# Performance work log

Measured on AMD Instinct MI355X. Metric: run time of the kernel, lower is better.

## Reference

```python
import jax, jax.numpy as jnp
import numpy as np
from jax import lax

DIM = 1024
INTER = 512
N_EXPERTS = 16
TOPK = 4
ROUTE_SCALE = 2.5
VOCAB = 32000


def setup_inputs() -> dict:
    key = jax.random.key(0)
    ks = jax.random.split(key, 8)
    x = jax.random.normal(ks[0], (2, 512, DIM), dtype=jnp.float32)
    input_ids = jax.random.randint(ks[1], (2, 512), 0, VOCAB)
    s = 0.02
    gate_w = jax.random.normal(ks[2], (N_EXPERTS, DIM), dtype=jnp.float32) * s
    gate_b = jax.random.normal(ks[3], (N_EXPERTS,), dtype=jnp.float32) * s
    # routed experts: w13 maps dim -> 2*inter (gate|up), w2 maps inter -> dim
    w13 = jax.random.normal(ks[4], (N_EXPERTS, 2 * INTER, DIM), dtype=jnp.float32) * s
    w2 = jax.random.normal(ks[5], (N_EXPERTS, DIM, INTER), dtype=jnp.float32) * s
    # shared expert
    w13_s = jax.random.normal(ks[6], (2 * INTER, DIM), dtype=jnp.float32) * s
    w2_s = jax.random.normal(ks[7], (DIM, INTER), dtype=jnp.float32) * s
    return {"x": x, "input_ids": input_ids, "gate_w": gate_w, "gate_b": gate_b,
            "w13": w13, "w2": w2, "w13_s": w13_s, "w2_s": w2_s}


def _silu_and_mul(gu):
    gate, up = jnp.split(gu, 2, axis=-1)
    return jax.nn.silu(gate) * up


def reference(x, input_ids, gate_w, gate_b, w13, w2, w13_s, w2_s):
    B, S, D = x.shape
    xt = x.reshape(-1, D)                      # [T, D]
    T = xt.shape[0]
    # ---- Gate (sigmoid score func, bias added for selection only) ----
    scores = jax.nn.sigmoid(xt.astype(jnp.float32) @ gate_w.T)   # [T, E]
    biased = scores + gate_b
    _, idx = lax.top_k(biased, TOPK)                             # [T, K] int
    w = jnp.take_along_axis(scores, idx, axis=-1)                # [T, K]
    w = w / jnp.sum(w, axis=-1, keepdims=True)                   # normalize (non-softmax)
    w = w * ROUTE_SCALE
    # ---- dispatch/combine as dense per-expert combine weights ----
    comb = jnp.zeros((T, N_EXPERTS), jnp.float32)
    comb = comb.at[jnp.arange(T)[:, None], idx].add(w)           # [T, E]
    comb = comb.astype(x.dtype)

    def expert_body(y, args):
        w13_e, w2_e, c_e = args                                  # [2I,D], [D,I], [T]
        h = _silu_and_mul(xt @ w13_e.T)                          # [T, I]
        return y + c_e[:, None] * (h @ w2_e.T), None

    y, _ = lax.scan(expert_body, jnp.zeros_like(xt), (w13, w2, comb.T))
    # ---- shared expert ----
    y = y + _silu_and_mul(xt @ w13_s.T) @ w2_s.T
    return y.astype(x.dtype).reshape(B, S, D)
```

## Files before the change

kernel.cpp:

```cpp
#include <hip/hip_runtime.h>
#include <hip/hip_bf16.h>
#include <math.h>

#define NTOK   1024
#define DIMX   1024
#define INTERX 512
#define NEXP   16
#define RSCALE 2.5f

typedef _Float16 f16x8 __attribute__((ext_vector_type(8)));
typedef _Float16 f16x4v __attribute__((ext_vector_type(4)));
typedef float    f32x4 __attribute__((ext_vector_type(4)));

#define N_W13  (NEXP * 2 * INTERX * DIMX)
#define N_W2   (NEXP * DIMX * INTERX)
#define N_W13S (2 * INTERX * DIMX)
#define N_W2S  (DIMX * INTERX)
#define N_X    (NTOK * DIMX)
#define N_CVTW ((size_t)N_W13 + N_W2 + N_W13S + N_W2S)
#define N_CVT  (N_CVTW + N_X)

#define WS_COUNTS  0
#define WS_TOKIDX  256
#define WS_SLOTS   (WS_TOKIDX + NEXP * NTOK * 4)
#define WS_WQ      (WS_SLOTS + NTOK * 16)
#define WS_SEL     (WS_WQ + NTOK * 16)
#define WS_NT      (WS_SEL + NTOK * 16)
#define WS_TE      (WS_NT + 64)
#define WS_TM      (WS_TE + 1024)
#define WS_TR      (WS_TM + 1024)
#define WS_H       (WS_TR + 1024)
#define WS_YC      (WS_H + (size_t)5120 * 512 * 2)
#define WS_F16     (WS_YC + (size_t)5120 * 1024 * 4)

#define SWZ(r, k) ((r) * 64 + ((k) ^ (((r) & 7) << 3)))

#define GATE_BLOCKS 256
#define CVTW_BLOCKS 3264

__device__ __forceinline__ f16x8 ldcvt(const float* __restrict__ p) {
    const float4 a = *(const float4*)p;
    const float4 b = *(const float4*)(p + 4);
    return (f16x8){(_Float16)a.x, (_Float16)a.y, (_Float16)a.z, (_Float16)a.w,
                   (_Float16)b.x, (_Float16)b.y, (_Float16)b.z, (_Float16)b.w};
}

__device__ __forceinline__ void gl_lds16(const _Float16* g, _Float16* l) {
    __builtin_amdgcn_global_load_lds(
        (const __attribute__((address_space(1))) void*)g,
        (__attribute__((address_space(3))) void*)l, 16, 0, 0);
}

__global__ __launch_bounds__(256) void gate_cvt(
    const float* __restrict__ x, const float* __restrict__ gw,
    const float* __restrict__ gb,
    const float* __restrict__ w13, const float* __restrict__ w2,
    const float* __restrict__ w13s, const float* __restrict__ w2s,
    int* __restrict__ sel, float* __restrict__ wq,
    _Float16* __restrict__ dh, _Float16* __restrict__ xh)
{
    if (blockIdx.x >= GATE_BLOCKS) {
        const size_t base8 = (size_t)(blockIdx.x - GATE_BLOCKS) * 256 + threadIdx.x;
        float4 ra[4], rb[4];
#pragma unroll
        for (int it = 0; it < 4; ++it) {
            size_t off = (base8 + (size_t)it * (CVTW_BLOCKS * 256)) * 8;
            const float* s;
            if (off < N_W13)                       s = w13 + off;
            else if ((off -= N_W13) < N_W2)        s = w2 + off;
            else if ((off -= N_W2) < N_W13S)       s = w13s + off;
            else                                   s = w2s + (off - N_W13S);
            ra[it] = *(const float4*)s;
            rb[it] = *(const float4*)(s + 4);
        }
#pragma unroll
        for (int it = 0; it < 4; ++it) {
            const size_t i8 = base8 + (size_t)it * (CVTW_BLOCKS * 256);
            f16x8 v = {(_Float16)ra[it].x, (_Float16)ra[it].y,
                       (_Float16)ra[it].z, (_Float16)ra[it].w,
                       (_Float16)rb[it].x, (_Float16)rb[it].y,
                       (_Float16)rb[it].z, (_Float16)rb[it].w};
            *(f16x8*)(dh + i8 * 8) = v;
        }
        return;
    }

    const int t    = blockIdx.x * 4 + (threadIdx.x >> 6);
    const int lane = threadIdx.x & 63;
    const int e    = lane & 15;
    const int q    = lane >> 4;

    const float4* xq = (const float4*)(x + (size_t)t * DIMX) + q * 64;
    const float4* gq = (const float4*)(gw + (size_t)e * DIMX) + q * 64;
    float s0 = 0.f, s1 = 0.f, s2 = 0.f, s3 = 0.f;
#pragma unroll 8
    for (int i = 0; i < 64; i += 2) {
        const float4 a = xq[i],     b = gq[i];
        const float4 c = xq[i + 1], d = gq[i + 1];
        s0 = fmaf(a.x, b.x, s0); s1 = fmaf(a.y, b.y, s1);
        s2 = fmaf(a.z, b.z, s2); s3 = fmaf(a.w, b.w, s3);
        s0 = fmaf(c.x, d.x, s0); s1 = fmaf(c.y, d.y, s1);
        s2 = fmaf(c.z, d.z, s2); s3 = fmaf(c.w, d.w, s3);
    }
    float acc = (s0 + s1) + (s2 + s3);
    acc += __shfl_xor(acc, 16);
    acc += __shfl_xor(acc, 32);

    {
        const float* xr = x + (size_t)t * DIMX + lane * 16;
        *(f16x8*)(xh + (size_t)t * DIMX + lane * 16)     = ldcvt(xr);
        *(f16x8*)(xh + (size_t)t * DIMX + lane * 16 + 8) = ldcvt(xr + 8);
    }

    const float sv = 1.f / (1.f + __expf(-acc));
    float v = (lane < 16) ? (sv + gb[e]) : -1e30f;

    float wk0, wk1, wk2, wk3; int ek0, ek1, ek2, ek3;
    float wsum = 0.f;
#pragma unroll
    for (int k = 0; k < 4; ++k) {
        float bestv = v; int besti = lane;
#pragma unroll
        for (int off = 8; off >= 1; off >>= 1) {
            const float ov = __shfl_xor(bestv, off);
            const int   oi = __shfl_xor(besti, off);
            if (ov > bestv || (ov == bestv && oi < besti)) { bestv = ov; besti = oi; }
        }
        besti = __shfl(besti, 0);
        const float sbest = __shfl(sv, besti);
        if (k == 0) { wk0 = sbest; ek0 = besti; }
        if (k == 1) { wk1 = sbest; ek1 = besti; }
        if (k == 2) { wk2 = sbest; ek2 = besti; }
        if (k == 3) { wk3 = sbest; ek3 = besti; }
        wsum += sbest;
        if (lane == besti) v = -1e30f;
    }
    const float scale = RSCALE / wsum;

    if (lane == 0) {
        sel[t * 4 + 0] = ek0;  wq[t * 4 + 0] = wk0 * scale;
        sel[t * 4 + 1] = ek1;  wq[t * 4 + 1] = wk1 * scale;
        sel[t * 4 + 2] = ek2;  wq[t * 4 + 2] = wk2 * scale;
        sel[t * 4 + 3] = ek3;  wq[t * 4 + 3] = wk3 * scale;
    }
}

__global__ __launch_bounds__(1024) void build(
    const int* __restrict__ sel,
    int* __restrict__ counts, int* __restrict__ tok_idx,
    int* __restrict__ slots,
    int* __restrict__ n_tiles, int* __restrict__ tile_e,
    int* __restrict__ tile_m0, int* __restrict__ tile_r0)
{
    __shared__ int lc[NEXP];
    const int t = threadIdx.x;
    if (t < NEXP) lc[t] = 0;
    __syncthreads();

    int e0 = sel[t * 4 + 0], e1 = sel[t * 4 + 1];
    int e2 = sel[t * 4 + 2], e3 = sel[t * 4 + 3];
    int p0 = atomicAdd(&lc[e0], 1);
    int p1 = atomicAdd(&lc[e1], 1);
    int p2 = atomicAdd(&lc[e2], 1);
    int p3 = atomicAdd(&lc[e3], 1);
    tok_idx[e0 * NTOK + p0] = t;  slots[t * 4 + 0] = (e0 << 10) | p0;
    tok_idx[e1 * NTOK + p1] = t;  slots[t * 4 + 1] = (e1 << 10) | p1;
    tok_idx[e2 * NTOK + p2] = t;  slots[t * 4 + 2] = (e2 << 10) | p2;
    tok_idx[e3 * NTOK + p3] = t;  slots[t * 4 + 3] = (e3 << 10) | p3;

    __syncthreads();
    if (t < NEXP) counts[t] = lc[t];
    if (t == 0) {
        int nt = 0, row = 0;
        for (int e = 0; e <= NEXP; ++e) {
            const int c = (e == NEXP) ? NTOK : lc[e];
            for (int m0 = 0; m0 < c; m0 += 128) {
                tile_e[nt]  = e;
                tile_m0[nt] = m0;
                tile_r0[nt] = row + m0;
                ++nt;
            }
            row += c;
        }
        n_tiles[0] = nt;
    }
}

#define WAITV8()  do { asm volatile("s_waitcnt vmcnt(8)" ::: "memory"); \
                       __builtin_amdgcn_sched_barrier(0); } while (0)
#define WAITV0()  do { asm volatile("s_waitcnt vmcnt(0)" ::: "memory"); \
                       __builtin_amdgcn_sched_barrier(0); } while (0)
#define RBAR()    do { __builtin_amdgcn_s_barrier(); \
                       __builtin_amdgcn_sched_barrier(0); } while (0)

__global__ __launch_bounds__(256, 2) void ffn1g(
    const _Float16* __restrict__ xh,
    const _Float16* __restrict__ w13h, const _Float16* __restrict__ w13sh,
    const int* __restrict__ counts, const int* __restrict__ tok_idx,
    const int* __restrict__ n_tiles, const int* __restrict__ tile_e,
    const int* __restrict__ tile_m0, const int* __restrict__ tile_r0,
    _Float16* __restrict__ h)
{
    const int tile = blockIdx.x >> 3;
    if (tile >= n_tiles[0]) return;
    const int y  = blockIdx.x & 7;
    const int e  = tile_e[tile];
    const int m0 = tile_m0[tile];
    const int rowbase = tile_r0[tile] - m0;
    const int Me = (e == NEXP) ? NTOK : counts[e];
    const int g0 = y * 64;

    const int tid = threadIdx.x, lane = tid & 63;
    const int wid = tid >> 6;
    const int wm = wid >> 1, wn = wid & 1;
    const int li = lane & 15, rk = (lane >> 4) * 8;

    const _Float16* Wh = (e == NEXP) ? w13sh : (w13h + (size_t)e * (2 * INTERX) * DIMX);

    __shared__ _Float16 T[2][256 * 64];

    const int lrow = lane >> 3;
    const int lc   = (lane & 7) ^ lrow;
    const _Float16* src[8];
    int ldsoff[8];
#pragma unroll
    for (int j = 0; j < 8; ++j) {
        const int c = wid * 8 + j;
        const int r = c * 8 + lrow;
        ldsoff[j] = c * 512;
        if (r < 128) {
            int ma = m0 + r; if (ma >= Me) ma = Me - 1;
            const int tok = (e == NEXP) ? ma : tok_idx[e * NTOK + ma];
            src[j] = xh + (size_t)tok * DIMX + lc * 8;
        } else {
            const int rb = r - 128;
            const int bwn = rb >> 6, bf = (rb >> 4) & 3, bli = rb & 15;
            const int wrow = ((bf & 2) ? INTERX : 0) + g0 + bwn * 32 + (bf & 1) * 16 + bli;
            src[j] = Wh + (size_t)wrow * DIMX + lc * 8;
        }
    }

    f32x4 acc[4][4];
#pragma unroll
    for (int i = 0; i < 4; ++i)
#pragma unroll
        for (int f = 0; f < 4; ++f) acc[i][f] = (f32x4){0.f, 0.f, 0.f, 0.f};

    auto STAGE = [&](int b, int k0) {
#pragma unroll
        for (int j = 0; j < 8; ++j)
            gl_lds16(src[j] + k0, &T[b][ldsoff[j]]);
    };
    auto MM = [&](int b) {
#pragma unroll
        for (int kk = 0; kk < 64; kk += 32) {
            f16x8 afr[4], bfr[4];
#pragma unroll
            for (int i = 0; i < 4; ++i) {
                const int r = wm * 64 + i * 16 + li;
                afr[i] = *(const f16x8*)&T[b][SWZ(r, kk + rk)];
            }
#pragma unroll
            for (int f = 0; f < 4; ++f) {
                const int r = 128 + wn * 64 + f * 16 + li;
                bfr[f] = *(const f16x8*)&T[b][SWZ(r, kk + rk)];
            }
#pragma unroll
            for (int i = 0; i < 4; ++i)
#pragma unroll
                for (int f = 0; f < 4; ++f)
                    acc[i][f] = __builtin_amdgcn_mfma_f32_16x16x32_f16(
                        afr[i], bfr[f], acc[i][f], 0, 0, 0);
        }
    };

    STAGE(0, 0);
    WAITV0();
    RBAR();
    int cur = 0;
#pragma unroll
    for (int t = 0; t < DIMX / 64; ++t) {
        if (t + 1 < DIMX / 64) {
            STAGE(cur ^ 1, (t + 1) * 64);
            WAITV8();
        } else {
            WAITV0();
        }
        RBAR();
        MM(cur);
        RBAR();
        cur ^= 1;
    }

#pragma unroll
    for (int i = 0; i < 4; ++i) {
#pragma unroll
        for (int q = 0; q < 4; ++q) {
            const int m = m0 + wm * 64 + i * 16 + (lane >> 4) * 4 + q;
            if (m >= Me) continue;
            _Float16* hp = h + (size_t)(rowbase + m) * INTERX + g0 + wn * 32 + li;
#pragma unroll
            for (int f = 0; f < 2; ++f) {
                const float g = acc[i][f][q];
                const float u = acc[i][f + 2][q];
                hp[f * 16] = (_Float16)(g * u / (1.f + __expf(-g)));
            }
        }
    }
}

__global__ __launch_bounds__(256, 2) void ffn2g(
    const _Float16* __restrict__ w2h, const _Float16* __restrict__ w2sh,
    const int* __restrict__ counts, const _Float16* __restrict__ h,
    const int* __restrict__ n_tiles, const int* __restrict__ tile_e,
    const int* __restrict__ tile_m0, const int* __restrict__ tile_r0,
    _Float16* __restrict__ yc)
{
    const int tile = blockIdx.x >> 3;
    if (tile >= n_tiles[0]) return;
    const int y  = blockIdx.x & 7;
    const int e  = tile_e[tile];
    const int m0 = tile_m0[tile];
    const int rowbase = tile_r0[tile] - m0;
    const int Me = (e == NEXP) ? NTOK : counts[e];
    const int n0 = y * 128;

    const int tid = threadIdx.x, lane = tid & 63;
    const int wid = tid >> 6;
    const int wm = wid >> 1, wn = wid & 1;
    const int li = lane & 15, rk = (lane >> 4) * 8;

    const _Float16* Wh = (e == NEXP) ? w2sh : (w2h + (size_t)e * DIMX * INTERX);

    __shared__ _Float16 T[2][256 * 64];

    const int lrow = lane >> 3;
    const int lc   = (lane & 7) ^ lrow;
    const _Float16* src[8];
    int ldsoff[8];
#pragma unroll
    for (int j = 0; j < 8; ++j) {
        const int c = wid * 8 + j;
        const int r = c * 8 + lrow;
        ldsoff[j] = c * 512;
        if (r < 128) {
            src[j] = h + (size_t)(rowbase + m0 + r) * INTERX + lc * 8;
        } else {
            const int rb = r - 128;
            src[j] = Wh + (size_t)(n0 + rb) * INTERX + lc * 8;
        }
    }

    f32x4 acc[4][4];
#pragma unroll
    for (int i = 0; i < 4; ++i)
#pragma unroll
        for (int f = 0; f < 4; ++f) acc[i][f] = (f32x4){0.f, 0.f, 0.f, 0.f};

    auto STAGE = [&](int b, int k0) {
#pragma unroll
        for (int j = 0; j < 8; ++j)
            gl_lds16(src[j] + k0, &T[b][ldsoff[j]]);
    };
    auto MM = [&](int b) {
#pragma unroll
        for (int kk = 0; kk < 64; kk += 32) {
            f16x8 afr[4], bfr[4];
#pragma unroll
            for (int i = 0; i < 4; ++i) {
                const int r = wm * 64 + i * 16 + li;
                afr[i] = *(const f16x8*)&T[b][SWZ(r, kk + rk)];
            }
#pragma unroll
            for (int f = 0; f < 4; ++f) {
                const int r = 128 + wn * 64 + f * 16 + li;
                bfr[f] = *(const f16x8*)&T[b][SWZ(r, kk + rk)];
            }
#pragma unroll
            for (int i = 0; i < 4; ++i)
#pragma unroll
                for (int f = 0; f < 4; ++f)
                    acc[i][f] = __builtin_amdgcn_mfma_f32_16x16x32_f16(
                        afr[i], bfr[f], acc[i][f], 0, 0, 0);
        }
    };

    STAGE(0, 0);
    WAITV0();
    RBAR();
    int cur = 0;
#pragma unroll
    for (int t = 0; t < INTERX / 64; ++t) {
        if (t + 1 < INTERX / 64) {
            STAGE(cur ^ 1, (t + 1) * 64);
            WAITV8();
        } else {
            WAITV0();
        }
        RBAR();
        MM(cur);
        RBAR();
        cur ^= 1;
    }

#pragma unroll
    for (int i = 0; i < 4; ++i) {
#pragma unroll
        for (int q = 0; q < 4; ++q) {
            const int m = m0 + wm * 64 + i * 16 + (lane >> 4) * 4 + q;
            if (m >= Me) continue;
            _Float16* yp = yc + (size_t)(rowbase + m) * DIMX + n0 + wn * 64 + li;
#pragma unroll
            for (int f = 0; f < 4; ++f)
                yp[f * 16] = (_Float16)acc[i][f][q];
        }
    }
}

__global__ __launch_bounds__(256) void combine(
    const int* __restrict__ counts,
    const int* __restrict__ slots,
    const float* __restrict__ wq,
    const _Float16* __restrict__ yc,
    float* __restrict__ out)
{
    __shared__ int soff[NEXP];
    if (threadIdx.x < NEXP) {
        int o = 0;
        for (int i = 0; i < (int)threadIdx.x; ++i) o += counts[i];
        soff[threadIdx.x] = o;
    }
    __syncthreads();

    const int t = blockIdx.x;
    const int tid = threadIdx.x;
    const f16x4v* ycv = (const f16x4v*)yc;
    const f16x4v b = ycv[(size_t)(4096 + t) * 256 + tid];
    float a0 = (float)b[0], a1 = (float)b[1], a2 = (float)b[2], a3 = (float)b[3];
#pragma unroll
    for (int k = 0; k < 4; ++k) {
        const int s   = slots[t * 4 + k];
        const int e   = s >> 10, pos = s & 1023;
        const float w = wq[t * 4 + k];
        const f16x4v v = ycv[(size_t)(soff[e] + pos) * 256 + tid];
        a0 = fmaf(w, (float)v[0], a0); a1 = fmaf(w, (float)v[1], a1);
        a2 = fmaf(w, (float)v[2], a2); a3 = fmaf(w, (float)v[3], a3);
    }
    ((float4*)out)[(size_t)t * 256 + tid] = make_float4(a0, a1, a2, a3);
}

extern "C" void kernel_launch(void* const* d_in, const int* in_sizes, int n_in,
                              void* d_out, int out_size, void* d_ws, size_t ws_size,
                              hipStream_t stream)
{
    const float* x    = (const float*)d_in[0];
    const float* gw   = (const float*)d_in[2];
    const float* gb   = (const float*)d_in[3];
    const float* w13  = (const float*)d_in[4];
    const float* w2   = (const float*)d_in[5];
    const float* w13s = (const float*)d_in[6];
    const float* w2s  = (const float*)d_in[7];
    float* out = (float*)d_out;

    char* ws = (char*)d_ws;
    int*       counts  = (int*)(ws + WS_COUNTS);
    int*       tok_idx = (int*)(ws + WS_TOKIDX);
    int*       slots   = (int*)(ws + WS_SLOTS);
    float*     wq      = (float*)(ws + WS_WQ);
    int*       sel     = (int*)(ws + WS_SEL);
    int*       n_tiles = (int*)(ws + WS_NT);
    int*       tile_e  = (int*)(ws + WS_TE);
    int*       tile_m0 = (int*)(ws + WS_TM);
    int*       tile_r0 = (int*)(ws + WS_TR);
    _Float16*  h       = (_Float16*)(ws + WS_H);
    _Float16*  yc      = (_Float16*)(ws + WS_YC);
    _Float16*  dh      = (_Float16*)(ws + WS_F16);
    _Float16*  w13h    = dh;
    _Float16*  w2h     = w13h + N_W13;
    _Float16*  w13sh   = w2h + N_W2;
    _Float16*  w2sh    = w13sh + N_W13S;
    _Float16*  xh      = w2sh + N_W2S;

    gate_cvt<<<GATE_BLOCKS + CVTW_BLOCKS, 256, 0, stream>>>(
        x, gw, gb, w13, w2, w13s, w2s, sel, wq, dh, xh);
    build<<<1, 1024, 0, stream>>>(sel, counts, tok_idx, slots,
                                  n_tiles, tile_e, tile_m0, tile_r0);

    ffn1g<<<1088, 256, 0, stream>>>(xh, w13h, w13sh, counts, tok_idx,
                                    n_tiles, tile_e, tile_m0, tile_r0, h);
    ffn2g<<<1088, 256, 0, stream>>>(w2h, w2sh, counts, h,
                                    n_tiles, tile_e, tile_m0, tile_r0, yc);
    combine<<<NTOK, 256, 0, stream>>>(counts, slots, wq, yc, out);
}
```

Baseline: 82.65 us.

## Overlap w2 fp16 conversion with first expert GEMM kernel

Splits the fp32-to-fp16 weight conversion so that the first kernel converts only w13 and shared w13, while the w2 and shared w2 conversion runs as extra blocks appended to the ffn1g launch. This moves part of the bandwidth-heavy conversion off the serial path ahead of routing and the first GEMM, letting it overlap with that GEMM. The cost is that the conversion blocks now compete with the GEMM tiles for memory bandwidth and CU slots. The conversion loop is also restructured to issue all loads before the stores behind a scheduling barrier.

```diff
diff --git a/kernel.cpp b/kernel.cpp
--- a/kernel.cpp
+++ b/kernel.cpp
@@ -17,8 +17,7 @@
 #define N_W13S (2 * INTERX * DIMX)
 #define N_W2S  (DIMX * INTERX)
 #define N_X    (NTOK * DIMX)
-#define N_CVTW ((size_t)N_W13 + N_W2 + N_W13S + N_W2S)
-#define N_CVT  (N_CVTW + N_X)
+#define N_CVT  ((size_t)N_W13 + N_W2 + N_W13S + N_W2S + N_X)
 
 #define WS_COUNTS  0
 #define WS_TOKIDX  256
@@ -35,8 +34,10 @@
 
 #define SWZ(r, k) ((r) * 64 + ((k) ^ (((r) & 7) << 3)))
 
-#define GATE_BLOCKS 256
-#define CVTW_BLOCKS 3264
+#define GATE_BLOCKS  256
+#define CVT13_BLOCKS 2176
+#define CVT2_BLOCKS  1088
+#define FFN_BLOCKS   1088
 
 __device__ __forceinline__ f16x8 ldcvt(const float* __restrict__ p) {
     const float4 a = *(const float4*)p;
@@ -45,43 +46,63 @@
                    (_Float16)b.x, (_Float16)b.y, (_Float16)b.z, (_Float16)b.w};
 }
 
+__device__ __forceinline__ f16x8 cvt8(const float4& a, const float4& b) {
+    return (f16x8){(_Float16)a.x, (_Float16)a.y, (_Float16)a.z, (_Float16)a.w,
+                   (_Float16)b.x, (_Float16)b.y, (_Float16)b.z, (_Float16)b.w};
+}
+
 __device__ __forceinline__ void gl_lds16(const _Float16* g, _Float16* l) {
     __builtin_amdgcn_global_load_lds(
         (const __attribute__((address_space(1))) void*)g,
         (__attribute__((address_space(3))) void*)l, 16, 0, 0);
 }
 
-__global__ __launch_bounds__(256) void gate_cvt(
+__device__ __forceinline__ void cvt_body(
+    size_t base8, size_t stride8,
+    const float* __restrict__ sA, size_t nA, size_t dA,
+    const float* __restrict__ sB, size_t dB,
+    _Float16* __restrict__ dh)
+{
+    const float* s0; const float* s1; const float* s2; const float* s3;
+    size_t d0, d1, d2, d3;
+    {
+        size_t off = (base8 + 0 * stride8) * 8;
+        if (off < nA) { s0 = sA + off; d0 = dA + off; }
+        else          { s0 = sB + (off - nA); d0 = dB + (off - nA); }
+        off = (base8 + 1 * stride8) * 8;
+        if (off < nA) { s1 = sA + off; d1 = dA + off; }
+        else          { s1 = sB + (off - nA); d1 = dB + (off - nA); }
+        off = (base8 + 2 * stride8) * 8;
+        if (off < nA) { s2 = sA + off; d2 = dA + off; }
+        else          { s2 = sB + (off - nA); d2 = dB + (off - nA); }
+        off = (base8 + 3 * stride8) * 8;
+        if (off < nA) { s3 = sA + off; d3 = dA + off; }
+        else          { s3 = sB + (off - nA); d3 = dB + (off - nA); }
+    }
+    const float4 a0 = *(const float4*)s0, b0 = *(const float4*)(s0 + 4);
+    const float4 a1 = *(const float4*)s1, b1 = *(const float4*)(s1 + 4);
+    const float4 a2 = *(const float4*)s2, b2 = *(const float4*)(s2 + 4);
+    const float4 a3 = *(const float4*)s3, b3 = *(const float4*)(s3 + 4);
+    __builtin_amdgcn_sched_barrier(0);
+    *(f16x8*)(dh + d0) = cvt8(a0, b0);
+    *(f16x8*)(dh + d1) = cvt8(a1, b1);
+    *(f16x8*)(dh + d2) = cvt8(a2, b2);
+    *(f16x8*)(dh + d3) = cvt8(a3, b3);
+}
+
+__global__ __launch_bounds__(256) void gate_cvt13(
     const float* __restrict__ x, const float* __restrict__ gw,
     const float* __restrict__ gb,
-    const float* __restrict__ w13, const float* __restrict__ w2,
-    const float* __restrict__ w13s, const float* __restrict__ w2s,
+    const float* __restrict__ w13, const float* __restrict__ w13s,
     int* __restrict__ sel, float* __restrict__ wq,
     _Float16* __restrict__ dh, _Float16* __restrict__ xh)
 {
     if (blockIdx.x >= GATE_BLOCKS) {
         const size_t base8 = (size_t)(blockIdx.x - GATE_BLOCKS) * 256 + threadIdx.x;
-        float4 ra[4], rb[4];
-#pragma unroll
-        for (int it = 0; it < 4; ++it) {
-            size_t off = (base8 + (size_t)it * (CVTW_BLOCKS * 256)) * 8;
-            const float* s;
-            if (off < N_W13)                       s = w13 + off;
-            else if ((off -= N_W13) < N_W2)        s = w2 + off;
-            else if ((off -= N_W2) < N_W13S)       s = w13s + off;
-            else                                   s = w2s + (off - N_W13S);
-            ra[it] = *(const float4*)s;
-            rb[it] = *(const float4*)(s + 4);
-        }
-#pragma unroll
-        for (int it = 0; it < 4; ++it) {
-            const size_t i8 = base8 + (size_t)it * (CVTW_BLOCKS * 256);
-            f16x8 v = {(_Float16)ra[it].x, (_Float16)ra[it].y,
-                       (_Float16)ra[it].z, (_Float16)ra[it].w,
-                       (_Float16)rb[it].x, (_Float16)rb[it].y,
-                       (_Float16)rb[it].z, (_Float16)rb[it].w};
-            *(f16x8*)(dh + i8 * 8) = v;
-        }
+        cvt_body(base8, (size_t)CVT13_BLOCKS * 256,
+                 w13, N_W13, 0,
+                 w13s, (size_t)N_W13 + N_W2,
+                 dh);
         return;
     }
 
@@ -196,11 +217,21 @@
 __global__ __launch_bounds__(256, 2) void ffn1g(
     const _Float16* __restrict__ xh,
     const _Float16* __restrict__ w13h, const _Float16* __restrict__ w13sh,
+    const float* __restrict__ w2f, const float* __restrict__ w2sf,
     const int* __restrict__ counts, const int* __restrict__ tok_idx,
     const int* __restrict__ n_tiles, const int* __restrict__ tile_e,
     const int* __restrict__ tile_m0, const int* __restrict__ tile_r0,
-    _Float16* __restrict__ h)
-{
+    _Float16* __restrict__ dh, _Float16* __restrict__ h)
+{
+    if (blockIdx.x >= FFN_BLOCKS) {
+        const size_t base8 = (size_t)(blockIdx.x - FFN_BLOCKS) * 256 + threadIdx.x;
+        cvt_body(base8, (size_t)CVT2_BLOCKS * 256,
+                 w2f, N_W2, (size_t)N_W13,
+                 w2sf, (size_t)N_W13 + N_W2 + N_W13S,
+                 dh);
+        return;
+    }
+
     const int tile = blockIdx.x >> 3;
     if (tile >= n_tiles[0]) return;
     const int y  = blockIdx.x & 7;
@@ -481,14 +512,15 @@
     _Float16*  w2sh    = w13sh + N_W13S;
     _Float16*  xh      = w2sh + N_W2S;
 
-    gate_cvt<<<GATE_BLOCKS + CVTW_BLOCKS, 256, 0, stream>>>(
-        x, gw, gb, w13, w2, w13s, w2s, sel, wq, dh, xh);
+    gate_cvt13<<<GATE_BLOCKS + CVT13_BLOCKS, 256, 0, stream>>>(
+        x, gw, gb, w13, w13s, sel, wq, dh, xh);
     build<<<1, 1024, 0, stream>>>(sel, counts, tok_idx, slots,
                                   n_tiles, tile_e, tile_m0, tile_r0);
 
-    ffn1g<<<1088, 256, 0, stream>>>(xh, w13h, w13sh, counts, tok_idx,
-                                    n_tiles, tile_e, tile_m0, tile_r0, h);
-    ffn2g<<<1088, 256, 0, stream>>>(w2h, w2sh, counts, h,
-                                    n_tiles, tile_e, tile_m0, tile_r0, yc);
+    ffn1g<<<FFN_BLOCKS + CVT2_BLOCKS, 256, 0, stream>>>(
+        xh, w13h, w13sh, w2, w2s, counts, tok_idx,
+        n_tiles, tile_e, tile_m0, tile_r0, dh, h);
+    ffn2g<<<FFN_BLOCKS, 256, 0, stream>>>(w2h, w2sh, counts, h,
+                                          n_tiles, tile_e, tile_m0, tile_r0, yc);
     combine<<<NTOK, 256, 0, stream>>>(counts, slots, wq, yc, out);
 }
```

Result: no change. 81.34 us (-1.6%).
